# Performance work log

Measured on AMD Instinct MI355X. Metric: run time of the kernel, lower is better.

## Reference

```python
import jax, jax.numpy as jnp
import numpy as np


def _lstm_layer(x, w_ih, w_hh, b_ih, b_hh):
    # x: [B,T,I]; w_ih: [4H,I]; w_hh: [4H,H]. PyTorch gate order: i,f,g,o.
    B, T, _ = x.shape
    H = w_hh.shape[1]
    xg = jnp.einsum('bti,gi->btg', x, w_ih) + b_ih  # precompute input gates [B,T,4H]

    def step(carry, xt):
        h, c = carry
        g = xt + h @ w_hh.T + b_hh
        i, f, gg, o = jnp.split(g, 4, axis=-1)
        c = jax.nn.sigmoid(f) * c + jax.nn.sigmoid(i) * jnp.tanh(gg)
        h = jax.nn.sigmoid(o) * jnp.tanh(c)
        return (h, c), h

    init = (jnp.zeros((B, H), x.dtype), jnp.zeros((B, H), x.dtype))
    _, hs = jax.lax.scan(step, init, jnp.swapaxes(xg, 0, 1))  # [T,B,H]
    return jnp.swapaxes(hs, 0, 1)


def _lstm2(x, p):  # 2-layer stacked LSTM; p = list of 2 layer param tuples
    for (wih, whh, bih, bhh) in p:
        x = _lstm_layer(x, wih, whh, bih, bhh)
    return x


def setup_inputs() -> dict:
    key = jax.random.key(0)
    ks = iter(jax.random.split(key, 32))
    d = {'x': jax.random.normal(next(ks), (100, 75, 75), jnp.float32)}
    specs = {
        'w_ih_1_0': (512, 75), 'w_hh_1_0': (512, 128), 'b_ih_1_0': (512,), 'b_hh_1_0': (512,),
        'w_ih_1_1': (512, 128), 'w_hh_1_1': (512, 128), 'b_ih_1_1': (512,), 'b_hh_1_1': (512,),
        'w_ih_2_0': (256, 128), 'w_hh_2_0': (256, 64), 'b_ih_2_0': (256,), 'b_hh_2_0': (256,),
        'w_ih_2_1': (256, 64), 'w_hh_2_1': (256, 64), 'b_ih_2_1': (256,), 'b_hh_2_1': (256,),
        'w_ih_3_0': (128, 64), 'w_hh_3_0': (128, 32), 'b_ih_3_0': (128,), 'b_hh_3_0': (128,),
        'w_ih_3_1': (128, 32), 'w_hh_3_1': (128, 32), 'b_ih_3_1': (128,), 'b_hh_3_1': (128,),
        'lin_w': (60, 2400), 'lin_b': (60,),
    }
    for name, shp in specs.items():
        d[name] = jax.random.normal(next(ks), shp, jnp.float32) * 0.1
    return d


def reference(x,
              w_ih_1_0, w_hh_1_0, b_ih_1_0, b_hh_1_0,
              w_ih_1_1, w_hh_1_1, b_ih_1_1, b_hh_1_1,
              w_ih_2_0, w_hh_2_0, b_ih_2_0, b_hh_2_0,
              w_ih_2_1, w_hh_2_1, b_ih_2_1, b_hh_2_1,
              w_ih_3_0, w_hh_3_0, b_ih_3_0, b_hh_3_0,
              w_ih_3_1, w_hh_3_1, b_ih_3_1, b_hh_3_1,
              lin_w, lin_b):
    x = _lstm2(x, [(w_ih_1_0, w_hh_1_0, b_ih_1_0, b_hh_1_0),
                   (w_ih_1_1, w_hh_1_1, b_ih_1_1, b_hh_1_1)])
    x = _lstm2(x, [(w_ih_2_0, w_hh_2_0, b_ih_2_0, b_hh_2_0),
                   (w_ih_2_1, w_hh_2_1, b_ih_2_1, b_hh_2_1)])
    x = _lstm2(x, [(w_ih_3_0, w_hh_3_0, b_ih_3_0, b_hh_3_0),
                   (w_ih_3_1, w_hh_3_1, b_ih_3_1, b_hh_3_1)])
    x = x.reshape((100, 32 * 75))  # [B, T*H] (row-major, matches torch)
    return x @ lin_w.T + lin_b
```

## Files before the change

kernel.cpp:

```cpp
#include <hip/hip_runtime.h>

using half8 = __attribute__((ext_vector_type(8))) _Float16;
using f32x4 = __attribute__((ext_vector_type(4))) float;

__device__ __forceinline__ float sigmf(float x) {
    return __builtin_amdgcn_rcpf(1.0f + __expf(-x));
}
__device__ __forceinline__ float tanhx(float x) {
    return 1.0f - 2.0f * __builtin_amdgcn_rcpf(1.0f + __expf(x + x));
}
__device__ __forceinline__ half8 cvt8(const float* p) {
    f32x4 a = *(const f32x4*)p;
    f32x4 b = *(const f32x4*)(p + 4);
    half8 r;
    r[0] = (_Float16)a[0]; r[1] = (_Float16)a[1];
    r[2] = (_Float16)a[2]; r[3] = (_Float16)a[3];
    r[4] = (_Float16)b[0]; r[5] = (_Float16)b[1];
    r[6] = (_Float16)b[2]; r[7] = (_Float16)b[3];
    return r;
}

__global__ __launch_bounds__(256) void prep_lw(const float* __restrict__ lw,
                                               _Float16* __restrict__ lwI) {
    int i = blockIdx.x * 256 + threadIdx.x;
    if (i >= 153600) return;
    int t = i >> 11;
    int rem = i & 2047;
    int tile = rem >> 9, op = (rem >> 5) & 15, hc = rem & 31;
    int o = tile * 16 + op;
    float v = (o < 60) ? lw[(size_t)o * 2400 + t * 32 + hc] : 0.0f;
    lwI[i] = (_Float16)v;
}

__global__ __launch_bounds__(256) void gemm_xg0(
    const float* __restrict__ X,
    const float* __restrict__ W0,
    const float* __restrict__ bi0, const float* __restrict__ bh0,
    float* __restrict__ C) {
    constexpr int Ks = 3, LDK = 104, HP = 48, N = 512;
    __shared__ __align__(16) _Float16 Al[64][LDK];
    __shared__ __align__(16) _Float16 Wl[64][LDK];

    const int tid = threadIdx.x;
    const int tt = blockIdx.x >> 1;
    const int boff = (blockIdx.x & 1) * 48;
    const int n0 = blockIdx.y * 64;

    for (int idx = tid; idx < 64 * HP; idx += 256) {
        int row = idx / HP;
        int k = (idx - row * HP) * 2;
        unsigned int va = 0, vw = 0;
        int b = boff + row;
        if (b < 100 && k < 75) {
            float f0 = X[((size_t)b * 75 + tt) * 75 + k];
            float f1 = (k + 1 < 75) ? X[((size_t)b * 75 + tt) * 75 + k + 1] : 0.0f;
            _Float16 h2[2] = {(_Float16)f0, (_Float16)f1};
            va = *(unsigned int*)h2;
        }
        if (k < 75) {
            int n = n0 + row;
            int src = (n & 3) * 128 + (n >> 2);
            float f0 = W0[(size_t)src * 75 + k];
            float f1 = (k + 1 < 75) ? W0[(size_t)src * 75 + k + 1] : 0.0f;
            _Float16 h2[2] = {(_Float16)f0, (_Float16)f1};
            vw = *(unsigned int*)h2;
        }
        *(unsigned int*)&Al[row][k] = va;
        *(unsigned int*)&Wl[row][k] = vw;
    }
    __syncthreads();

    const int w = tid >> 6, l = tid & 63, hi = l >> 4;
    half8 a[Ks];
    #pragma unroll
    for (int kk = 0; kk < Ks; ++kk)
        a[kk] = *(const half8*)&Al[w * 16 + (l & 15)][kk * 32 + hi * 8];

    f32x4 acc[4];
    #pragma unroll
    for (int jt = 0; jt < 4; ++jt) {
        acc[jt] = f32x4{0.f, 0.f, 0.f, 0.f};
        #pragma unroll
        for (int kk = 0; kk < Ks; ++kk) {
            half8 b = *(const half8*)&Wl[jt * 16 + (l & 15)][kk * 32 + hi * 8];
            acc[jt] = __builtin_amdgcn_mfma_f32_16x16x32_f16(a[kk], b, acc[jt], 0, 0, 0);
        }
    }

    const int bx = (boff >> 2) + w * 4 + hi;
    #pragma unroll
    for (int jt = 0; jt < 4; ++jt) {
        int n = n0 + jt * 16 + (l & 15);
        int src = (n & 3) * 128 + (n >> 2);
        float bs = bi0[src] + bh0[src];
        f32x4 v = acc[jt];
        v[0] += bs; v[1] += bs; v[2] += bs; v[3] += bs;
        *(f32x4*)(C + ((size_t)(tt * 28 + bx) * N + n) * 4) = v;
    }
}

__global__ __launch_bounds__(256) void gemm_xg1(
    const _Float16* __restrict__ A,
    const float* __restrict__ W1,
    const float* __restrict__ bi1, const float* __restrict__ bh1,
    float* __restrict__ C) {
    constexpr int Ks = 4, LDK = 136, HP = 64, Kv = 128, N = 512;
    __shared__ __align__(16) _Float16 Al[64][LDK];
    __shared__ __align__(16) _Float16 Wl[64][LDK];

    const int tid = threadIdx.x;
    const int tt = blockIdx.x >> 1;
    const int boff = (blockIdx.x & 1) * 48;
    const int n0 = blockIdx.y * 64;

    for (int idx = tid; idx < 64 * HP; idx += 256) {
        int row = idx / HP;
        int k = (idx - row * HP) * 2;
        unsigned int va = *(const unsigned int*)(A + (size_t)(tt * 112 + boff + row) * Kv + k);
        int n = n0 + row;
        int src = (n & 3) * 128 + (n >> 2);
        float f0 = W1[(size_t)src * 128 + k];
        float f1 = W1[(size_t)src * 128 + k + 1];
        _Float16 h2[2] = {(_Float16)f0, (_Float16)f1};
        *(unsigned int*)&Al[row][k] = va;
        *(unsigned int*)&Wl[row][k] = *(unsigned int*)h2;
    }
    __syncthreads();

    const int w = tid >> 6, l = tid & 63, hi = l >> 4;
    half8 a[Ks];
    #pragma unroll
    for (int kk = 0; kk < Ks; ++kk)
        a[kk] = *(const half8*)&Al[w * 16 + (l & 15)][kk * 32 + hi * 8];

    f32x4 acc[4];
    #pragma unroll
    for (int jt = 0; jt < 4; ++jt) {
        acc[jt] = f32x4{0.f, 0.f, 0.f, 0.f};
        #pragma unroll
        for (int kk = 0; kk < Ks; ++kk) {
            half8 b = *(const half8*)&Wl[jt * 16 + (l & 15)][kk * 32 + hi * 8];
            acc[jt] = __builtin_amdgcn_mfma_f32_16x16x32_f16(a[kk], b, acc[jt], 0, 0, 0);
        }
    }

    const int bx = (boff >> 2) + w * 4 + hi;
    #pragma unroll
    for (int jt = 0; jt < 4; ++jt) {
        int n = n0 + jt * 16 + (l & 15);
        int src = (n & 3) * 128 + (n >> 2);
        float bs = bi1[src] + bh1[src];
        f32x4 v = acc[jt];
        v[0] += bs; v[1] += bs; v[2] += bs; v[3] += bs;
        *(f32x4*)(C + ((size_t)(tt * 28 + bx) * N + n) * 4) = v;
    }
}

#define FTAIL                                                                 \
    __builtin_amdgcn_sched_barrier(0);                                        \
    asm volatile("s_waitcnt lgkmcnt(0)");                                     \
    __builtin_amdgcn_sched_barrier(0);                                        \
    __builtin_amdgcn_s_barrier();                                             \
    __builtin_amdgcn_sched_barrier(0);

#define PICK(A4) ((hi & 2) ? ((hi & 1) ? A4[3] : A4[2]) : ((hi & 1) ? A4[1] : A4[0]))

#define ACT(aI, aF, aG4, aO)                                                  \
    float gI = PICK(aI), gF = PICK(aF), gG = PICK(aG4), gO = PICK(aO);        \
    float si = sigmf(gI), sf = sigmf(gF), tg = tanhx(gG), so = sigmf(gO);     \
    float cn = sf * cst + si * tg;                                            \
    cst = cn;                                                                 \
    float hn = so * tanhx(cn);                                                \
    _Float16 hv = (_Float16)hn;

__global__ __launch_bounds__(512, 2) void lstm_rec0(
    const float* __restrict__ xg,
    const float* __restrict__ whhf,
    _Float16* __restrict__ hout) {
    constexpr int H = 128, Ks = 4, LDH = 160;
    constexpr int XSTR = 448 * H;
    constexpr int HSTR = 112 * H;

    __shared__ __align__(16) _Float16 hbuf[2][4][LDH];

    const int tid = threadIdx.x;
    const int w = tid >> 6, l = tid & 63, hi = l >> 4;
    const int col = w * 16 + (l & 15);
    const int blk = blockIdx.x;

    half8 bw[4][Ks];
    #pragma unroll
    for (int G = 0; G < 4; ++G)
        #pragma unroll
        for (int kk = 0; kk < Ks; ++kk)
            bw[G][kk] = cvt8(whhf + (size_t)(G * H + col) * H + kk * 32 + hi * 8);

    for (int i = tid; i < 2 * 4 * LDH; i += 512) ((_Float16*)hbuf)[i] = (_Float16)0;
    __syncthreads();

    const float* xp = xg + (size_t)blk * (4 * H * 4) + col * 16;
    _Float16* hop = hout + (size_t)(blk * 4 + hi) * H + col;

    f32x4 P0[4], P1[4], P2[4];
#define XLOAD(PA)                                                             \
    PA[0] = *(const f32x4*)(xp + 0);                                          \
    PA[1] = *(const f32x4*)(xp + 4);                                          \
    PA[2] = *(const f32x4*)(xp + 8);                                          \
    PA[3] = *(const f32x4*)(xp + 12);                                         \
    xp += XSTR;

    XLOAD(P0)
    XLOAD(P1)
    XLOAD(P2)

    float cst = 0.f;

#define LSTM_STEP(PA, CUR)                                                    \
    {                                                                         \
        half8 afr[Ks];                                                        \
        _Pragma("unroll") for (int kk = 0; kk < Ks; ++kk)                     \
            afr[kk] = *(const half8*)&hbuf[CUR][(l & 15) & 3][kk * 32 + hi * 8]; \
        f32x4 aI = PA[0], aF = PA[1], aG4 = PA[2], aO = PA[3];                \
        XLOAD(PA)                                                             \
        _Pragma("unroll") for (int kk = 0; kk < Ks; ++kk) {                   \
            aI = __builtin_amdgcn_mfma_f32_16x16x32_f16(afr[kk], bw[0][kk], aI, 0, 0, 0);  \
            aF = __builtin_amdgcn_mfma_f32_16x16x32_f16(afr[kk], bw[1][kk], aF, 0, 0, 0);  \
            aG4 = __builtin_amdgcn_mfma_f32_16x16x32_f16(afr[kk], bw[2][kk], aG4, 0, 0, 0);\
            aO = __builtin_amdgcn_mfma_f32_16x16x32_f16(afr[kk], bw[3][kk], aO, 0, 0, 0);  \
        }                                                                     \
        ACT(aI, aF, aG4, aO)                                                  \
        hbuf[CUR ^ 1][hi][col] = hv;                                          \
        *hop = hv;                                                            \
        hop += HSTR;                                                          \
        FTAIL                                                                 \
    }

    #pragma unroll 1
    for (int it = 0; it < 12; ++it) {
        LSTM_STEP(P0, 0) LSTM_STEP(P1, 1) LSTM_STEP(P2, 0)
        LSTM_STEP(P0, 1) LSTM_STEP(P1, 0) LSTM_STEP(P2, 1)
    }
    LSTM_STEP(P0, 0) LSTM_STEP(P1, 1) LSTM_STEP(P2, 0)
#undef LSTM_STEP
#undef XLOAD
}

__global__ __launch_bounds__(768, 3) void rec1xg(
    const float* __restrict__ xg1,
    const float* __restrict__ whh1f,
    const float* __restrict__ wih2f,
    const float* __restrict__ bi2, const float* __restrict__ bh2,
    float* __restrict__ xg2) {
    constexpr int H = 128, Ks = 4, LDH = 160;
    constexpr int XSTR = 448 * H;

    __shared__ __align__(16) _Float16 hb1[2][4][LDH];
    __shared__ __align__(16) _Float16 hp[2][4][LDH];

    const int tid = threadIdx.x;
    const int w = tid >> 6, l = tid & 63, hi = l >> 4;
    const int lr = (l & 15) & 3;
    const int blk = blockIdx.x;

    for (int i = tid; i < 2 * 4 * LDH; i += 768) {
        ((_Float16*)hb1)[i] = (_Float16)0;
        ((_Float16*)hp)[i] = (_Float16)0;
    }
    __syncthreads();

    float cst = 0.f;

    if (w < 8) {
        const int col = w * 16 + (l & 15);
        half8 bw[4][Ks];
        #pragma unroll
        for (int G = 0; G < 4; ++G)
            #pragma unroll
            for (int kk = 0; kk < Ks; ++kk)
                bw[G][kk] = cvt8(whh1f + (size_t)(G * H + col) * H + kk * 32 + hi * 8);

        const float* xp = xg1 + (size_t)blk * (4 * H * 4) + col * 16;
        f32x4 P0[4], P1[4];
#define XLOADA(PA)                                                            \
        PA[0] = *(const f32x4*)(xp + 0);                                      \
        PA[1] = *(const f32x4*)(xp + 4);                                      \
        PA[2] = *(const f32x4*)(xp + 8);                                      \
        PA[3] = *(const f32x4*)(xp + 12);                                     \
        xp += XSTR;
        XLOADA(P0)
        XLOADA(P1)

#define ASTEP(PA, CUR)                                                        \
        {                                                                     \
            half8 afr[Ks];                                                    \
            _Pragma("unroll") for (int kk = 0; kk < Ks; ++kk)                 \
                afr[kk] = *(const half8*)&hb1[CUR][lr][kk * 32 + hi * 8];     \
            f32x4 aI = PA[0], aF = PA[1], aG4 = PA[2], aO = PA[3];            \
            XLOADA(PA)                                                        \
            _Pragma("unroll") for (int kk = 0; kk < Ks; ++kk) {               \
                aI = __builtin_amdgcn_mfma_f32_16x16x32_f16(afr[kk], bw[0][kk], aI, 0, 0, 0);  \
                aF = __builtin_amdgcn_mfma_f32_16x16x32_f16(afr[kk], bw[1][kk], aF, 0, 0, 0);  \
                aG4 = __builtin_amdgcn_mfma_f32_16x16x32_f16(afr[kk], bw[2][kk], aG4, 0, 0, 0);\
                aO = __builtin_amdgcn_mfma_f32_16x16x32_f16(afr[kk], bw[3][kk], aO, 0, 0, 0);  \
            }                                                                 \
            ACT(aI, aF, aG4, aO)                                              \
            hb1[(CUR) ^ 1][hi][col] = hv;                                     \
            hp[(CUR) ^ 1][hi][col] = hv;                                      \
        }

        #pragma unroll 1
        for (int it = 0; it < 38; ++it) {
            ASTEP(P0, 0)
            FTAIL
            if (2 * it + 1 < 75) { ASTEP(P1, 1) }
            FTAIL
        }
#undef ASTEP
#undef XLOADA
    } else {
        const int col = (w - 8) * 16 + (l & 15);
        half8 bwI[4][Ks];
        #pragma unroll
        for (int G = 0; G < 4; ++G)
            #pragma unroll
            for (int kk = 0; kk < Ks; ++kk)
                bwI[G][kk] = cvt8(wih2f + (size_t)(G * 64 + col) * 128 + kk * 32 + hi * 8);
        float bb[4];
        #pragma unroll
        for (int G = 0; G < 4; ++G) bb[G] = bi2[G * 64 + col] + bh2[G * 64 + col];
        float* xq = xg2 + (size_t)blk * 1024 + col * 16;

        #pragma unroll 1
        for (int s = 0; s < 76; ++s) {
            const int cur = s & 1;
            if (s >= 1) {
                half8 air[Ks];
                #pragma unroll
                for (int kk = 0; kk < Ks; ++kk)
                    air[kk] = *(const half8*)&hp[cur][lr][kk * 32 + hi * 8];
                f32x4 acc[4];
                #pragma unroll
                for (int G = 0; G < 4; ++G)
                    acc[G] = f32x4{bb[G], bb[G], bb[G], bb[G]};
                #pragma unroll
                for (int G = 0; G < 4; ++G)
                    #pragma unroll
                    for (int kk = 0; kk < Ks; ++kk)
                        acc[G] = __builtin_amdgcn_mfma_f32_16x16x32_f16(air[kk], bwI[G][kk], acc[G], 0, 0, 0);
                if (hi == 0) {
                    #pragma unroll
                    for (int G = 0; G < 4; ++G)
                        *(f32x4*)(xq + (size_t)(s - 1) * 28672 + G * 4) = acc[G];
                }
            }
            FTAIL
        }
    }
}

struct QuadPtrs {
    const float* xg;
    const float* whh2;
    const float* whh3;
    const float* wih3;
    const float* whh4;
    const float* wih4;
    const float* whh5;
    const float* wih5;
    const float* bi3; const float* bh3;
    const float* bi4; const float* bh4;
    const float* bi5; const float* bh5;
    const _Float16* lwI;
    const float* lb;
    float* outF;
};

__global__ __launch_bounds__(832) void lstm_quad(QuadPtrs q) {
    __shared__ __align__(16) _Float16 hb2[2][4][96], hp2[2][4][96];
    __shared__ __align__(16) _Float16 hb3[2][4][96], hp3[2][4][96];
    __shared__ __align__(16) _Float16 hb4[2][4][80], hp4[2][4][80];
    __shared__ __align__(16) _Float16 hb5[2][4][80];

    const int tid = threadIdx.x;
    const int w = tid >> 6, l = tid & 63, hi = l >> 4;
    const int lr = (l & 15) & 3;
    const int blk = blockIdx.x;

    for (int i = tid; i < 2 * 4 * 96; i += 832) {
        ((_Float16*)hb2)[i] = (_Float16)0; ((_Float16*)hp2)[i] = (_Float16)0;
        ((_Float16*)hb3)[i] = (_Float16)0; ((_Float16*)hp3)[i] = (_Float16)0;
    }
    for (int i = tid; i < 2 * 4 * 80; i += 832) {
        ((_Float16*)hb4)[i] = (_Float16)0; ((_Float16*)hp4)[i] = (_Float16)0;
        ((_Float16*)hb5)[i] = (_Float16)0;
    }
    __syncthreads();

    float cst = 0.f;

    if (w < 4) {
        const int col = w * 16 + (l & 15);
        half8 bw[4][2];
        #pragma unroll
        for (int G = 0; G < 4; ++G)
            #pragma unroll
            for (int kk = 0; kk < 2; ++kk)
                bw[G][kk] = cvt8(q.whh2 + (size_t)(G * 64 + col) * 64 + kk * 32 + hi * 8);
        const float* xp = q.xg + (size_t)blk * 1024 + col * 16;
        f32x4 P0[4], P1[4], P2[4];
#define XLOADQ(PA)                                                            \
        PA[0] = *(const f32x4*)(xp + 0);                                      \
        PA[1] = *(const f32x4*)(xp + 4);                                      \
        PA[2] = *(const f32x4*)(xp + 8);                                      \
        PA[3] = *(const f32x4*)(xp + 12);                                     \
        xp += 28672;
        XLOADQ(P0)
        XLOADQ(P1)
        XLOADQ(P2)

#define QA(PA, CUR, S)                                                        \
        {                                                                     \
            if ((S) < 75) {                                                   \
                half8 afr[2];                                                 \
                _Pragma("unroll") for (int kk = 0; kk < 2; ++kk)              \
                    afr[kk] = *(const half8*)&hb2[CUR][lr][kk * 32 + hi * 8]; \
                f32x4 aI = PA[0], aF = PA[1], aG4 = PA[2], aO = PA[3];        \
                XLOADQ(PA)                                                    \
                _Pragma("unroll") for (int kk = 0; kk < 2; ++kk) {            \
                    aI = __builtin_amdgcn_mfma_f32_16x16x32_f16(afr[kk], bw[0][kk], aI, 0, 0, 0);  \
                    aF = __builtin_amdgcn_mfma_f32_16x16x32_f16(afr[kk], bw[1][kk], aF, 0, 0, 0);  \
                    aG4 = __builtin_amdgcn_mfma_f32_16x16x32_f16(afr[kk], bw[2][kk], aG4, 0, 0, 0);\
                    aO = __builtin_amdgcn_mfma_f32_16x16x32_f16(afr[kk], bw[3][kk], aO, 0, 0, 0);  \
                }                                                             \
                ACT(aI, aF, aG4, aO)                                          \
                hb2[(CUR) ^ 1][hi][col] = hv;                                 \
                hp2[(CUR) ^ 1][hi][col] = hv;                                 \
            }                                                                 \
            FTAIL                                                             \
        }
        #pragma unroll 1
        for (int it = 0; it < 13; ++it) {
            const int b6 = it * 6;
            QA(P0, 0, b6 + 0) QA(P1, 1, b6 + 1) QA(P2, 0, b6 + 2)
            QA(P0, 1, b6 + 3) QA(P1, 0, b6 + 4) QA(P2, 1, b6 + 5)
        }
#undef QA
#undef XLOADQ
    } else if (w < 8) {
        const int col = (w - 4) * 16 + (l & 15);
        half8 bwB[4][2], bwI[4][2];
        #pragma unroll
        for (int G = 0; G < 4; ++G)
            #pragma unroll
            for (int kk = 0; kk < 2; ++kk) {
                bwB[G][kk] = cvt8(q.whh3 + (size_t)(G * 64 + col) * 64 + kk * 32 + hi * 8);
                bwI[G][kk] = cvt8(q.wih3 + (size_t)(G * 64 + col) * 64 + kk * 32 + hi * 8);
            }
        const float bI = q.bi3[col] + q.bh3[col];
        const float bF = q.bi3[64 + col] + q.bh3[64 + col];
        const float bG = q.bi3[128 + col] + q.bh3[128 + col];
        const float bO = q.bi3[192 + col] + q.bh3[192 + col];
        #pragma unroll 1
        for (int s = 0; s < 78; ++s) {
            const int cur = s & 1;
            if (s >= 1 && s <= 75) {
                half8 afr[2], air[2];
                #pragma unroll
                for (int kk = 0; kk < 2; ++kk) {
                    afr[kk] = *(const half8*)&hb3[cur][lr][kk * 32 + hi * 8];
                    air[kk] = *(const half8*)&hp2[cur][lr][kk * 32 + hi * 8];
                }
                f32x4 aI = {bI, bI, bI, bI}, aF = {bF, bF, bF, bF};
                f32x4 aG4 = {bG, bG, bG, bG}, aO = {bO, bO, bO, bO};
                #pragma unroll
                for (int kk = 0; kk < 2; ++kk) {
                    aI = __builtin_amdgcn_mfma_f32_16x16x32_f16(afr[kk], bwB[0][kk], aI, 0, 0, 0);
                    aF = __builtin_amdgcn_mfma_f32_16x16x32_f16(afr[kk], bwB[1][kk], aF, 0, 0, 0);
                    aG4 = __builtin_amdgcn_mfma_f32_16x16x32_f16(afr[kk], bwB[2][kk], aG4, 0, 0, 0);
                    aO = __builtin_amdgcn_mfma_f32_16x16x32_f16(afr[kk], bwB[3][kk], aO, 0, 0, 0);
                }
                #pragma unroll
                for (int kk = 0; kk < 2; ++kk) {
                    aI = __builtin_amdgcn_mfma_f32_16x16x32_f16(air[kk], bwI[0][kk], aI, 0, 0, 0);
                    aF = __builtin_amdgcn_mfma_f32_16x16x32_f16(air[kk], bwI[1][kk], aF, 0, 0, 0);
                    aG4 = __builtin_amdgcn_mfma_f32_16x16x32_f16(air[kk], bwI[2][kk], aG4, 0, 0, 0);
                    aO = __builtin_amdgcn_mfma_f32_16x16x32_f16(air[kk], bwI[3][kk], aO, 0, 0, 0);
                }
                ACT(aI, aF, aG4, aO)
                hb3[cur ^ 1][hi][col] = hv;
                hp3[cur ^ 1][hi][col] = hv;
            }
            FTAIL
        }
    } else if (w < 10) {
        const int col = (w - 8) * 16 + (l & 15);
        half8 bwB[4], bwI[4][2];
        #pragma unroll
        for (int G = 0; G < 4; ++G) {
            bwB[G] = cvt8(q.whh4 + (size_t)(G * 32 + col) * 32 + hi * 8);
            #pragma unroll
            for (int kk = 0; kk < 2; ++kk)
                bwI[G][kk] = cvt8(q.wih4 + (size_t)(G * 32 + col) * 64 + kk * 32 + hi * 8);
        }
        const float bI = q.bi4[col] + q.bh4[col];
        const float bF = q.bi4[32 + col] + q.bh4[32 + col];
        const float bG = q.bi4[64 + col] + q.bh4[64 + col];
        const float bO = q.bi4[96 + col] + q.bh4[96 + col];
        #pragma unroll 1
        for (int s = 0; s < 78; ++s) {
            const int cur = s & 1;
            if (s >= 2 && s <= 76) {
                half8 afr = *(const half8*)&hb4[cur][lr][hi * 8];
                half8 air[2];
                #pragma unroll
                for (int kk = 0; kk < 2; ++kk)
                    air[kk] = *(const half8*)&hp3[cur][lr][kk * 32 + hi * 8];
                f32x4 aI = {bI, bI, bI, bI}, aF = {bF, bF, bF, bF};
                f32x4 aG4 = {bG, bG, bG, bG}, aO = {bO, bO, bO, bO};
                aI = __builtin_amdgcn_mfma_f32_16x16x32_f16(afr, bwB[0], aI, 0, 0, 0);
                aF = __builtin_amdgcn_mfma_f32_16x16x32_f16(afr, bwB[1], aF, 0, 0, 0);
                aG4 = __builtin_amdgcn_mfma_f32_16x16x32_f16(afr, bwB[2], aG4, 0, 0, 0);
                aO = __builtin_amdgcn_mfma_f32_16x16x32_f16(afr, bwB[3], aO, 0, 0, 0);
                #pragma unroll
                for (int kk = 0; kk < 2; ++kk) {
                    aI = __builtin_amdgcn_mfma_f32_16x16x32_f16(air[kk], bwI[0][kk], aI, 0, 0, 0);
                    aF = __builtin_amdgcn_mfma_f32_16x16x32_f16(air[kk], bwI[1][kk], aF, 0, 0, 0);
                    aG4 = __builtin_amdgcn_mfma_f32_16x16x32_f16(air[kk], bwI[2][kk], aG4, 0, 0, 0);
                    aO = __builtin_amdgcn_mfma_f32_16x16x32_f16(air[kk], bwI[3][kk], aO, 0, 0, 0);
                }
                ACT(aI, aF, aG4, aO)
                hb4[cur ^ 1][hi][col] = hv;
                hp4[cur ^ 1][hi][col] = hv;
            }
            FTAIL
        }
    } else if (w < 12) {
        const int col = (w - 10) * 16 + (l & 15);
        half8 bwB[4], bwI[4];
        #pragma unroll
        for (int G = 0; G < 4; ++G) {
            bwB[G] = cvt8(q.whh5 + (size_t)(G * 32 + col) * 32 + hi * 8);
            bwI[G] = cvt8(q.wih5 + (size_t)(G * 32 + col) * 32 + hi * 8);
        }
        const float bI = q.bi5[col] + q.bh5[col];
        const float bF = q.bi5[32 + col] + q.bh5[32 + col];
        const float bG = q.bi5[64 + col] + q.bh5[64 + col];
        const float bO = q.bi5[96 + col] + q.bh5[96 + col];
        #pragma unroll 1
        for (int s = 0; s < 78; ++s) {
            const int cur = s & 1;
            if (s >= 3) {
                half8 afr = *(const half8*)&hb5[cur][lr][hi * 8];
                half8 air = *(const half8*)&hp4[cur][lr][hi * 8];
                f32x4 aI = {bI, bI, bI, bI}, aF = {bF, bF, bF, bF};
                f32x4 aG4 = {bG, bG, bG, bG}, aO = {bO, bO, bO, bO};
                aI = __builtin_amdgcn_mfma_f32_16x16x32_f16(afr, bwB[0], aI, 0, 0, 0);
                aF = __builtin_amdgcn_mfma_f32_16x16x32_f16(afr, bwB[1], aF, 0, 0, 0);
                aG4 = __builtin_amdgcn_mfma_f32_16x16x32_f16(afr, bwB[2], aG4, 0, 0, 0);
                aO = __builtin_amdgcn_mfma_f32_16x16x32_f16(afr, bwB[3], aO, 0, 0, 0);
                aI = __builtin_amdgcn_mfma_f32_16x16x32_f16(air, bwI[0], aI, 0, 0, 0);
                aF = __builtin_amdgcn_mfma_f32_16x16x32_f16(air, bwI[1], aF, 0, 0, 0);
                aG4 = __builtin_amdgcn_mfma_f32_16x16x32_f16(air, bwI[2], aG4, 0, 0, 0);
                aO = __builtin_amdgcn_mfma_f32_16x16x32_f16(air, bwI[3], aO, 0, 0, 0);
                ACT(aI, aF, aG4, aO)
                hb5[cur ^ 1][hi][col] = hv;
            }
            FTAIL
        }
    } else {
        const int ln = l & 15;
        const _Float16* lwp = q.lwI + (size_t)ln * 32 + hi * 8;
        half8 LA[4], LB[4];
        #pragma unroll
        for (int tl = 0; tl < 4; ++tl) {
            LA[tl] = *(const half8*)(lwp + (size_t)(0 * 4 + tl) * 512);
            LB[tl] = *(const half8*)(lwp + (size_t)(1 * 4 + tl) * 512);
        }
        f32x4 acc[4];
        #pragma unroll
        for (int tl = 0; tl < 4; ++tl) acc[tl] = f32x4{0.f, 0.f, 0.f, 0.f};

        #pragma unroll 1
        for (int it = 0; it < 39; ++it) {
            {
                int t = 2 * it - 4;
                if (t >= 0) {
                    half8 hf = *(const half8*)&hb5[0][lr][hi * 8];
                    #pragma unroll
                    for (int tl = 0; tl < 4; ++tl)
                        acc[tl] = __builtin_amdgcn_mfma_f32_16x16x32_f16(LA[tl], hf, acc[tl], 0, 0, 0);
                }
                int tn = t + 2;
                if (tn < 0) tn = 0;
                if (tn > 74) tn = 74;
                #pragma unroll
                for (int tl = 0; tl < 4; ++tl)
                    LA[tl] = *(const half8*)(lwp + ((size_t)tn * 4 + tl) * 512);
                FTAIL
            }
            {
                int t = 2 * it - 3;
                if (t >= 0) {
                    half8 hf = *(const half8*)&hb5[1][lr][hi * 8];
                    #pragma unroll
                    for (int tl = 0; tl < 4; ++tl)
                        acc[tl] = __builtin_amdgcn_mfma_f32_16x16x32_f16(LB[tl], hf, acc[tl], 0, 0, 0);
                }
                int tn = t + 2;
                if (tn < 0) tn = 0;
                if (tn > 74) tn = 74;
                #pragma unroll
                for (int tl = 0; tl < 4; ++tl)
                    LB[tl] = *(const half8*)(lwp + ((size_t)tn * 4 + tl) * 512);
                FTAIL
            }
        }
        {
            half8 hf = *(const half8*)&hb5[0][lr][hi * 8];
            #pragma unroll
            for (int tl = 0; tl < 4; ++tl)
                acc[tl] = __builtin_amdgcn_mfma_f32_16x16x32_f16(LA[tl], hf, acc[tl], 0, 0, 0);
        }
        if (ln < 4) {
            int b = blk * 4 + ln;
            #pragma unroll
            for (int tl = 0; tl < 4; ++tl)
                #pragma unroll
                for (int r = 0; r < 4; ++r) {
                    int o = tl * 16 + hi * 4 + r;
                    if (o < 60) q.outF[b * 60 + o] = acc[tl][r] + q.lb[o];
                }
        }
    }
}

extern "C" void kernel_launch(void* const* d_in, const int* in_sizes, int n_in,
                              void* d_out, int out_size, void* d_ws, size_t ws_size,
                              hipStream_t stream) {
    const float* x = (const float*)d_in[0];
    const float* wih[6];
    const float* whhp[6];
    const float* bih[6];
    const float* bhh[6];
    for (int i = 0; i < 6; ++i) {
        wih[i] = (const float*)d_in[1 + 4 * i];
        whhp[i] = (const float*)d_in[2 + 4 * i];
        bih[i] = (const float*)d_in[3 + 4 * i];
        bhh[i] = (const float*)d_in[4 + 4 * i];
    }
    const float* lw = (const float*)d_in[25];
    const float* lb = (const float*)d_in[26];
    float* out = (float*)d_out;

    char* ws = (char*)d_ws;
    size_t cur = 0;
    auto alloc = [&](size_t b) {
        size_t o = cur;
        cur += (b + 255) & ~(size_t)255;
        return o;
    };
    _Float16* lwI = (_Float16*)(ws + alloc(153600 * 2));
    float* xgA = (float*)(ws + alloc((size_t)78 * 28 * 512 * 4 * 4));
    float* xgB = (float*)(ws + alloc((size_t)78 * 28 * 256 * 4 * 4));
    _Float16* h0 = (_Float16*)(ws + alloc((size_t)75 * 112 * 128 * 2));

    prep_lw<<<600, 256, 0, stream>>>(lw, lwI);

    gemm_xg0<<<dim3(150, 8), 256, 0, stream>>>(x, wih[0], bih[0], bhh[0], xgA);
    lstm_rec0<<<25, 512, 0, stream>>>(xgA, whhp[0], h0);
    gemm_xg1<<<dim3(150, 8), 256, 0, stream>>>(h0, wih[1], bih[1], bhh[1], xgA);
    rec1xg<<<25, 768, 0, stream>>>(xgA, whhp[1], wih[2], bih[2], bhh[2], xgB);
    QuadPtrs q;
    q.xg = xgB;
    q.whh2 = whhp[2]; q.whh3 = whhp[3]; q.wih3 = wih[3];
    q.whh4 = whhp[4]; q.wih4 = wih[4]; q.whh5 = whhp[5]; q.wih5 = wih[5];
    q.bi3 = bih[3]; q.bh3 = bhh[3];
    q.bi4 = bih[4]; q.bh4 = bhh[4];
    q.bi5 = bih[5]; q.bh5 = bhh[5];
    q.lwI = lwI; q.lb = lb; q.outF = out;
    lstm_quad<<<25, 832, 0, stream>>>(q);
}
```

Measured before the change: 212.1 us.

## Unfuse layer-2 input projection from recurrence and pre-convert recurrent weights to fp16

Removes the fused rec1xg kernel, which ran the layer-1 recurrence on 8 waves while 4 extra waves computed the next layer's input gates step by step. Layer 1 now reuses the plain recurrence kernel, and the next layer's input projection runs afterwards as a separate parallel GEMM through a templated gemm_xgN. Recurrent weights for the first two layers are converted to fp16 once in a merged prep kernel, so the recurrence kernels load half8 directly instead of converting in place. The launch-bounds occupancy hint on the recurrence kernel is also dropped. This adds a kernel launch and a round trip of h1 through global memory, but takes the per-step projection MFMAs and the extra waves out of the serial critical path.

After: 185.3 us. -12.6%, faster.

```diff
diff --git a/kernel.cpp b/kernel.cpp
--- a/kernel.cpp
+++ b/kernel.cpp
@@ -20,16 +20,24 @@
     return r;
 }
 
-__global__ __launch_bounds__(256) void prep_lw(const float* __restrict__ lw,
-                                               _Float16* __restrict__ lwI) {
+__global__ __launch_bounds__(256) void prep_kernel(
+    const float* __restrict__ lw, const float* __restrict__ whh0,
+    const float* __restrict__ whh1, _Float16* __restrict__ lwI,
+    _Float16* __restrict__ wH0, _Float16* __restrict__ wH1) {
     int i = blockIdx.x * 256 + threadIdx.x;
-    if (i >= 153600) return;
-    int t = i >> 11;
-    int rem = i & 2047;
-    int tile = rem >> 9, op = (rem >> 5) & 15, hc = rem & 31;
-    int o = tile * 16 + op;
-    float v = (o < 60) ? lw[(size_t)o * 2400 + t * 32 + hc] : 0.0f;
-    lwI[i] = (_Float16)v;
+    if (i < 153600) {
+        int t = i >> 11;
+        int rem = i & 2047;
+        int tile = rem >> 9, op = (rem >> 5) & 15, hc = rem & 31;
+        int o = tile * 16 + op;
+        float v = (o < 60) ? lw[(size_t)o * 2400 + t * 32 + hc] : 0.0f;
+        lwI[i] = (_Float16)v;
+        return;
+    }
+    i -= 153600;
+    if (i < 65536) { wH0[i] = (_Float16)whh0[i]; return; }
+    i -= 65536;
+    if (i < 65536) { wH1[i] = (_Float16)whh1[i]; return; }
 }
 
 __global__ __launch_bounds__(256) void gemm_xg0(
@@ -99,12 +107,13 @@
     }
 }
 
-__global__ __launch_bounds__(256) void gemm_xg1(
+template <int HO>
+__global__ __launch_bounds__(256) void gemm_xgN(
     const _Float16* __restrict__ A,
-    const float* __restrict__ W1,
-    const float* __restrict__ bi1, const float* __restrict__ bh1,
+    const float* __restrict__ Wf,
+    const float* __restrict__ bi, const float* __restrict__ bh,
     float* __restrict__ C) {
-    constexpr int Ks = 4, LDK = 136, HP = 64, Kv = 128, N = 512;
+    constexpr int Ks = 4, LDK = 136, HP = 64, Kv = 128, N = 4 * HO;
     __shared__ __align__(16) _Float16 Al[64][LDK];
     __shared__ __align__(16) _Float16 Wl[64][LDK];
 
@@ -118,9 +127,9 @@
         int k = (idx - row * HP) * 2;
         unsigned int va = *(const unsigned int*)(A + (size_t)(tt * 112 + boff + row) * Kv + k);
         int n = n0 + row;
-        int src = (n & 3) * 128 + (n >> 2);
-        float f0 = W1[(size_t)src * 128 + k];
-        float f1 = W1[(size_t)src * 128 + k + 1];
+        int src = (n & 3) * HO + (n >> 2);
+        float f0 = Wf[(size_t)src * 128 + k];
+        float f1 = Wf[(size_t)src * 128 + k + 1];
         _Float16 h2[2] = {(_Float16)f0, (_Float16)f1};
         *(unsigned int*)&Al[row][k] = va;
         *(unsigned int*)&Wl[row][k] = *(unsigned int*)h2;
@@ -148,8 +157,8 @@
     #pragma unroll
     for (int jt = 0; jt < 4; ++jt) {
         int n = n0 + jt * 16 + (l & 15);
-        int src = (n & 3) * 128 + (n >> 2);
-        float bs = bi1[src] + bh1[src];
+        int src = (n & 3) * HO + (n >> 2);
+        float bs = bi[src] + bh[src];
         f32x4 v = acc[jt];
         v[0] += bs; v[1] += bs; v[2] += bs; v[3] += bs;
         *(f32x4*)(C + ((size_t)(tt * 28 + bx) * N + n) * 4) = v;
@@ -173,9 +182,9 @@
     float hn = so * tanhx(cn);                                                \
     _Float16 hv = (_Float16)hn;
 
-__global__ __launch_bounds__(512, 2) void lstm_rec0(
+__global__ __launch_bounds__(512) void lstm_rec(
     const float* __restrict__ xg,
-    const float* __restrict__ whhf,
+    const _Float16* __restrict__ whh,
     _Float16* __restrict__ hout) {
     constexpr int H = 128, Ks = 4, LDH = 160;
     constexpr int XSTR = 448 * H;
@@ -193,7 +202,7 @@
     for (int G = 0; G < 4; ++G)
         #pragma unroll
         for (int kk = 0; kk < Ks; ++kk)
-            bw[G][kk] = cvt8(whhf + (size_t)(G * H + col) * H + kk * 32 + hi * 8);
+            bw[G][kk] = *(const half8*)(whh + (size_t)(G * H + col) * H + kk * 32 + hi * 8);
 
     for (int i = tid; i < 2 * 4 * LDH; i += 512) ((_Float16*)hbuf)[i] = (_Float16)0;
     __syncthreads();
@@ -243,119 +252,6 @@
     LSTM_STEP(P0, 0) LSTM_STEP(P1, 1) LSTM_STEP(P2, 0)
 #undef LSTM_STEP
 #undef XLOAD
-}
-
-__global__ __launch_bounds__(768, 3) void rec1xg(
-    const float* __restrict__ xg1,
-    const float* __restrict__ whh1f,
-    const float* __restrict__ wih2f,
-    const float* __restrict__ bi2, const float* __restrict__ bh2,
-    float* __restrict__ xg2) {
-    constexpr int H = 128, Ks = 4, LDH = 160;
-    constexpr int XSTR = 448 * H;
-
-    __shared__ __align__(16) _Float16 hb1[2][4][LDH];
-    __shared__ __align__(16) _Float16 hp[2][4][LDH];
-
-    const int tid = threadIdx.x;
-    const int w = tid >> 6, l = tid & 63, hi = l >> 4;
-    const int lr = (l & 15) & 3;
-    const int blk = blockIdx.x;
-
-    for (int i = tid; i < 2 * 4 * LDH; i += 768) {
-        ((_Float16*)hb1)[i] = (_Float16)0;
-        ((_Float16*)hp)[i] = (_Float16)0;
-    }
-    __syncthreads();
-
-    float cst = 0.f;
-
-    if (w < 8) {
-        const int col = w * 16 + (l & 15);
-        half8 bw[4][Ks];
-        #pragma unroll
-        for (int G = 0; G < 4; ++G)
-            #pragma unroll
-            for (int kk = 0; kk < Ks; ++kk)
-                bw[G][kk] = cvt8(whh1f + (size_t)(G * H + col) * H + kk * 32 + hi * 8);
-
-        const float* xp = xg1 + (size_t)blk * (4 * H * 4) + col * 16;
-        f32x4 P0[4], P1[4];
-#define XLOADA(PA)                                                            \
-        PA[0] = *(const f32x4*)(xp + 0);                                      \
-        PA[1] = *(const f32x4*)(xp + 4);                                      \
-        PA[2] = *(const f32x4*)(xp + 8);                                      \
-        PA[3] = *(const f32x4*)(xp + 12);                                     \
-        xp += XSTR;
-        XLOADA(P0)
-        XLOADA(P1)
-
-#define ASTEP(PA, CUR)                                                        \
-        {                                                                     \
-            half8 afr[Ks];                                                    \
-            _Pragma("unroll") for (int kk = 0; kk < Ks; ++kk)                 \
-                afr[kk] = *(const half8*)&hb1[CUR][lr][kk * 32 + hi * 8];     \
-            f32x4 aI = PA[0], aF = PA[1], aG4 = PA[2], aO = PA[3];            \
-            XLOADA(PA)                                                        \
-            _Pragma("unroll") for (int kk = 0; kk < Ks; ++kk) {               \
-                aI = __builtin_amdgcn_mfma_f32_16x16x32_f16(afr[kk], bw[0][kk], aI, 0, 0, 0);  \
-                aF = __builtin_amdgcn_mfma_f32_16x16x32_f16(afr[kk], bw[1][kk], aF, 0, 0, 0);  \
-                aG4 = __builtin_amdgcn_mfma_f32_16x16x32_f16(afr[kk], bw[2][kk], aG4, 0, 0, 0);\
-                aO = __builtin_amdgcn_mfma_f32_16x16x32_f16(afr[kk], bw[3][kk], aO, 0, 0, 0);  \
-            }                                                                 \
-            ACT(aI, aF, aG4, aO)                                              \
-            hb1[(CUR) ^ 1][hi][col] = hv;                                     \
-            hp[(CUR) ^ 1][hi][col] = hv;                                      \
-        }
-
-        #pragma unroll 1
-        for (int it = 0; it < 38; ++it) {
-            ASTEP(P0, 0)
-            FTAIL
-            if (2 * it + 1 < 75) { ASTEP(P1, 1) }
-            FTAIL
-        }
-#undef ASTEP
-#undef XLOADA
-    } else {
-        const int col = (w - 8) * 16 + (l & 15);
-        half8 bwI[4][Ks];
-        #pragma unroll
-        for (int G = 0; G < 4; ++G)
-            #pragma unroll
-            for (int kk = 0; kk < Ks; ++kk)
-                bwI[G][kk] = cvt8(wih2f + (size_t)(G * 64 + col) * 128 + kk * 32 + hi * 8);
-        float bb[4];
-        #pragma unroll
-        for (int G = 0; G < 4; ++G) bb[G] = bi2[G * 64 + col] + bh2[G * 64 + col];
-        float* xq = xg2 + (size_t)blk * 1024 + col * 16;
-
-        #pragma unroll 1
-        for (int s = 0; s < 76; ++s) {
-            const int cur = s & 1;
-            if (s >= 1) {
-                half8 air[Ks];
-                #pragma unroll
-                for (int kk = 0; kk < Ks; ++kk)
-                    air[kk] = *(const half8*)&hp[cur][lr][kk * 32 + hi * 8];
-                f32x4 acc[4];
-                #pragma unroll
-                for (int G = 0; G < 4; ++G)
-                    acc[G] = f32x4{bb[G], bb[G], bb[G], bb[G]};
-                #pragma unroll
-                for (int G = 0; G < 4; ++G)
-                    #pragma unroll
-                    for (int kk = 0; kk < Ks; ++kk)
-                        acc[G] = __builtin_amdgcn_mfma_f32_16x16x32_f16(air[kk], bwI[G][kk], acc[G], 0, 0, 0);
-                if (hi == 0) {
-                    #pragma unroll
-                    for (int G = 0; G < 4; ++G)
-                        *(f32x4*)(xq + (size_t)(s - 1) * 28672 + G * 4) = acc[G];
-                }
-            }
-            FTAIL
-        }
-    }
 }
 
 struct QuadPtrs {
@@ -660,16 +556,20 @@
         return o;
     };
     _Float16* lwI = (_Float16*)(ws + alloc(153600 * 2));
+    _Float16* wH0 = (_Float16*)(ws + alloc(65536 * 2));
+    _Float16* wH1 = (_Float16*)(ws + alloc(65536 * 2));
     float* xgA = (float*)(ws + alloc((size_t)78 * 28 * 512 * 4 * 4));
     float* xgB = (float*)(ws + alloc((size_t)78 * 28 * 256 * 4 * 4));
     _Float16* h0 = (_Float16*)(ws + alloc((size_t)75 * 112 * 128 * 2));
-
-    prep_lw<<<600, 256, 0, stream>>>(lw, lwI);
+    _Float16* h1 = (_Float16*)(ws + alloc((size_t)75 * 112 * 128 * 2));
+
+    prep_kernel<<<1112, 256, 0, stream>>>(lw, whhp[0], whhp[1], lwI, wH0, wH1);
 
     gemm_xg0<<<dim3(150, 8), 256, 0, stream>>>(x, wih[0], bih[0], bhh[0], xgA);
-    lstm_rec0<<<25, 512, 0, stream>>>(xgA, whhp[0], h0);
-    gemm_xg1<<<dim3(150, 8), 256, 0, stream>>>(h0, wih[1], bih[1], bhh[1], xgA);
-    rec1xg<<<25, 768, 0, stream>>>(xgA, whhp[1], wih[2], bih[2], bhh[2], xgB);
+    lstm_rec<<<25, 512, 0, stream>>>(xgA, wH0, h0);
+    gemm_xgN<128><<<dim3(150, 8), 256, 0, stream>>>(h0, wih[1], bih[1], bhh[1], xgA);
+    lstm_rec<<<25, 512, 0, stream>>>(xgA, wH1, h1);
+    gemm_xgN<64><<<dim3(150, 4), 256, 0, stream>>>(h1, wih[2], bih[2], bhh[2], xgB);
     QuadPtrs q;
     q.xg = xgB;
     q.whh2 = whhp[2]; q.whh3 = whhp[3]; q.wih3 = wih[3];
```
